# Performance work log

Measured on AMD Instinct MI355X. Metric: run time of the kernel, lower is better.

The kernel has to match this reference:

```python
import jax, jax.numpy as jnp
from jax import lax
import numpy as np

DN = ('NCHW', 'OIHW', 'NCHW')
NUM_CLASSES = 80
TOPK = 100
EPS = 1e-6


def seek_local_maximum(x, eps=EPS):
    # x: [b, c, h, w]; 8-neighbor local-max with zero padding, like the torch code
    xp = jnp.pad(x, ((0, 0), (0, 0), (1, 1), (1, 1)))
    m = ((x >= xp[:, :, :-2, 1:-1]) & (x >= xp[:, :, 2:, 1:-1])
         & (x >= xp[:, :, 1:-1, :-2]) & (x >= xp[:, :, 1:-1, 2:])
         & (x >= xp[:, :, :-2, :-2]) & (x >= xp[:, :, :-2, 2:])
         & (x >= xp[:, :, 2:, :-2]) & (x >= xp[:, :, 2:, 2:])
         & (x >= eps))
    return m.astype(x.dtype)


def setup_inputs() -> dict:
    key = jax.random.key(0)
    k1, k2, k3, k4 = jax.random.split(key, 4)
    b, c, h, w = 8, 256, 100, 152
    nc1 = NUM_CLASSES + 1
    x = jax.random.normal(k1, (b, c, h, w), dtype=jnp.float32)
    pos_embeddings = jax.random.normal(k2, (1, c, h, w), dtype=jnp.float32)
    w1 = jax.random.normal(k3, (c, c, 3, 3), dtype=jnp.float32) * 0.02
    b1 = jnp.zeros((c,), dtype=jnp.float32)
    w2 = jax.random.normal(k4, (nc1, c, 1, 1), dtype=jnp.float32) * 0.02
    b2 = jnp.zeros((nc1,), dtype=jnp.float32)
    return {"x": x, "pos_embeddings": pos_embeddings, "w1": w1, "b1": b1, "w2": w2, "b2": b2}


def reference(x, pos_embeddings, w1, b1, w2, b2):
    b, c, h, w = x.shape
    # conv 3x3 + relu + conv 1x1 -> class logits [b, nc+1, h, w]
    hid = lax.conv_general_dilated(x, w1, (1, 1), 'SAME', dimension_numbers=DN)
    hid = jax.nn.relu(hid + b1[None, :, None, None])
    logits = lax.conv_general_dilated(hid, w2, (1, 1), 'SAME', dimension_numbers=DN)
    logits = logits + b2[None, :, None, None]
    probs = jax.nn.softmax(logits, axis=1)
    # one-hot of argmax over foreground classes (excluding last 'no-object' channel)
    cls_idx = jnp.argmax(probs[:, :-1], axis=1)                    # [b, h, w]
    one_hot = jax.nn.one_hot(cls_idx, NUM_CLASSES + 1, dtype=probs.dtype)  # [b, h, w, nc+1]
    probs = probs * jnp.transpose(one_hot, (0, 3, 1, 2))
    probs = probs + seek_local_maximum(probs)
    # per-pixel foreground score, topk over spatial positions
    scores = jnp.max(probs[:, :-1], axis=1).reshape(b, h * w)      # [b, h*w]
    _, topk_idx = lax.top_k(scores, TOPK)                          # [b, topk]
    idx = topk_idx[:, None, :]                                     # [b, 1, topk]
    topk_proposals = jnp.take_along_axis(x.reshape(b, c, h * w), idx, axis=2)
    pos = jnp.broadcast_to(pos_embeddings, (b, c, h, w)).reshape(b, c, h * w)
    topk_pos_embeddings = jnp.take_along_axis(pos, idx, axis=2)
    # eval mode: topk_locations is None in the torch module; omit it
    return (topk_proposals, topk_pos_embeddings, logits)
```

## Files before the change

kernel.cpp:

```cpp
#include <hip/hip_runtime.h>
#include <hip/hip_bf16.h>

#define Hh    100
#define Ww    152
#define Pp    15200
#define Cc    256
#define NBATCH 8
#define NC1   81
#define NCLS  80
#define KTOP  100

#define PROWS 102
#define PCOLS 154
#define PIXB  1024
#define XT_BATCH_BYTES ((size_t)PROWS * PCOLS * PIXB)

typedef __attribute__((ext_vector_type(8))) short  bf16x8;
typedef __attribute__((ext_vector_type(4))) float  f32x4;

__device__ __forceinline__ unsigned short bf16_bits(float v) {
    __hip_bfloat16 h = __float2bfloat16(v);
    return *(unsigned short*)&h;
}
__device__ __forceinline__ float bf16_back(float v) {
    __hip_bfloat16 h = __float2bfloat16(v);
    return __bfloat162float(h);
}

typedef __attribute__((address_space(1))) const void GV;
typedef __attribute__((address_space(3))) void LV;
__device__ __forceinline__ void gload_lds16(const void* g, void* l) {
    __builtin_amdgcn_global_load_lds((GV*)g, (LV*)l, 16, 0, 0);
}

__global__ void pack_w(const float* __restrict__ w1, unsigned short* __restrict__ wpk)
{
    int id = blockIdx.x * 256 + threadIdx.x;
    int k = id >> 8, c = id & 255;
#pragma unroll
    for (int t = 0; t < 9; ++t) {
        float v = w1[(size_t)(k * 256 + c) * 9 + t];
        unsigned short hi = bf16_bits(v);
        unsigned short lo = bf16_bits(v - bf16_back(v));
        int region = ((c >> 5) * 9 + t) * 2;
        int base   = region * 8192;
        int pos    = (k >> 4) * 512 + ((c >> 3) & 3) * 128 + (k & 15) * 8 + (c & 7);
        wpk[base + pos]        = hi;
        wpk[base + 8192 + pos] = lo;
    }
}

__global__ void pack_w2t(const float* __restrict__ w2, float* __restrict__ w2t)
{
    int j = blockIdx.x;
    int c = threadIdx.x;
    float v = (j < NC1) ? w2[j * 256 + c] : 0.f;
    w2t[c * 84 + j] = v;
}

__global__ __launch_bounds__(256)
void pack_x(const float* __restrict__ x, unsigned short* __restrict__ xT)
{
    __shared__ float ls[64][257];
    const int tid   = threadIdx.x;
    const int chunk = blockIdx.x;
    const int row   = blockIdx.y;
    const int n     = blockIdx.z;
    const int c0    = chunk * 64;
    const int yy    = row - 1;
    const bool rowok = ((unsigned)yy < (unsigned)Hh);

    const int lanec = tid & 63;
    const int xx    = c0 + lanec - 1;
    const bool colok = ((unsigned)xx < (unsigned)Ww);
    const bool ok = rowok && colok;

    const size_t rbase = ((size_t)n * Cc) * Pp + (size_t)(rowok ? yy : 0) * Ww
                       + (size_t)(colok ? xx : 0);
#pragma unroll 4
    for (int i = 0; i < 64; ++i) {
        const int c = (tid >> 6) + i * 4;
        float v = 0.f;
        if (ok) v = x[rbase + (size_t)c * Pp];
        ls[lanec][c] = v;
    }
    __syncthreads();

    const int cch = tid;
    const int jmax = (c0 + 64 <= PCOLS) ? 64 : (PCOLS - c0);
#pragma unroll 4
    for (int j = 0; j < jmax; ++j) {
        const int pc = c0 + j;
        float v = ls[j][cch];
        unsigned short hi = bf16_bits(v);
        unsigned short lo = bf16_bits(v - bf16_back(v));
        size_t dst = (((size_t)n * PROWS + row) * PCOLS + pc) * 512 + cch;
        xT[dst]       = hi;
        xT[dst + 256] = lo;
    }
}

#define BBUFB 49152

#define MM(P,M,I,CUR) acc[M][I] = __builtin_amdgcn_mfma_f32_16x16x32_bf16( \
    (P)==2 ? al[CUR][M] : ah[CUR][M], (P)==1 ? bl[CUR][I] : bh[CUR][I], acc[M][I], 0, 0, 0);

#define CH0(C) MM(0,0,0,C) MM(0,0,1,C) MM(0,0,2,C) MM(0,0,3,C) MM(0,1,0,C) MM(0,1,1,C) \
               MM(0,1,2,C) MM(0,1,3,C) MM(0,2,0,C) MM(0,2,1,C) MM(0,2,2,C) MM(0,2,3,C)
#define CH1(C) MM(0,3,0,C) MM(0,3,1,C) MM(0,3,2,C) MM(0,3,3,C) MM(1,0,0,C) MM(1,0,1,C) \
               MM(1,0,2,C) MM(1,0,3,C) MM(1,1,0,C) MM(1,1,1,C) MM(1,1,2,C) MM(1,1,3,C)
#define CH2(C) MM(1,2,0,C) MM(1,2,1,C) MM(1,2,2,C) MM(1,2,3,C) MM(1,3,0,C) MM(1,3,1,C) \
               MM(1,3,2,C) MM(1,3,3,C) MM(2,0,0,C) MM(2,0,1,C) MM(2,0,2,C) MM(2,0,3,C)
#define CH3(C) MM(2,1,0,C) MM(2,1,1,C) MM(2,1,2,C) MM(2,1,3,C) MM(2,2,0,C) MM(2,2,1,C) \
               MM(2,2,2,C) MM(2,2,3,C) MM(2,3,0,C) MM(2,3,1,C) MM(2,3,2,C) MM(2,3,3,C)

#define SBAR __builtin_amdgcn_sched_barrier(0)

#define TAP(S,T,CUR,NX) { \
    const int U_  = (S) * 9 + (T); \
    const int un_ = (U_ + 1 < 72) ? U_ + 1 : 71; \
    loadAh(un_, ah[NX]); \
    SBAR; __builtin_amdgcn_s_setprio(1); CH0(CUR) __builtin_amdgcn_s_setprio(0); SBAR; \
    loadAl(un_, al[NX]); \
    SBAR; __builtin_amdgcn_s_setprio(1); CH1(CUR) __builtin_amdgcn_s_setprio(0); SBAR; \
    if ((T) < 8) readBh((S), (T) + 1, bh[NX]); \
    SBAR; __builtin_amdgcn_s_setprio(1); CH2(CUR) __builtin_amdgcn_s_setprio(0); SBAR; \
    if ((T) < 8) readBl((S), (T) + 1, bl[NX]); \
    SBAR; __builtin_amdgcn_s_setprio(1); CH3(CUR) __builtin_amdgcn_s_setprio(0); SBAR; \
}

#define TAPS_EVEN(S) TAP(S,0,0,1) TAP(S,1,1,0) TAP(S,2,0,1) TAP(S,3,1,0) TAP(S,4,0,1) \
                     TAP(S,5,1,0) TAP(S,6,0,1) TAP(S,7,1,0) TAP(S,8,0,1)
#define TAPS_ODD(S)  TAP(S,0,1,0) TAP(S,1,0,1) TAP(S,2,1,0) TAP(S,3,0,1) TAP(S,4,1,0) \
                     TAP(S,5,0,1) TAP(S,6,1,0) TAP(S,7,0,1) TAP(S,8,1,0)

__global__ __launch_bounds__(512, 2)
void conv3x3_mfma(const unsigned short* __restrict__ xT,
                  const unsigned short* __restrict__ wpk,
                  const float* __restrict__ b1, float* __restrict__ hid)
{
    __shared__ f32x4 ldsbuf[6144];
    char* L = (char*)ldsbuf;

    const int tid  = threadIdx.x;
    const int lane = tid & 63;
    const int wv   = tid >> 6;
    const int wm   = wv >> 2;
    const int wn   = wv & 3;
    const int quad = lane >> 4, lq = lane & 15;

    const int hwflat  = blockIdx.x + 65 * (blockIdx.y + 2 * blockIdx.z);
    const int logical = (hwflat & 7) * 130 + (hwflat >> 3);
    const int n   = logical / 130;
    const int rem = logical - n * 130;
    const int bx  = rem >> 1;
    const int k0b = rem & 1;

    const int rb = bx / 5, cb = bx - rb * 5;
    const int y0 = rb * 8;
    const int x0 = cb * 32;
    const int k0 = k0b * 128;

    const char* xb = (const char*)xT + (size_t)n * XT_BATCH_BYTES;
    const char* abase = (const char*)wpk + (size_t)(k0 >> 4) * 1024
                      + (size_t)(wm * 4) * 1024 + (size_t)lane * 16;

    const unsigned kslot = (lane & 7) ^ (lane >> 3);
    const size_t chnbase = (kslot < 4) ? (size_t)(kslot * 16)
                                       : (size_t)(448 + kslot * 16);

    auto stageB = [&](int s) {
        char* bdst = L + (size_t)(s & 1) * BBUFB;
        const size_t chn = (size_t)s * 64 + chnbase;
#pragma unroll
        for (int k6 = 0; k6 < 6; ++k6) {
            const int j   = wv + 8 * k6;
            const int pix = 8 * j + (lane >> 3);
            const int r   = pix / 34;
            const int c   = pix - r * 34;
            int prow = y0 + r; prow = prow < 102 ? prow : 101;
            const char* g = xb + (((size_t)(prow * 154 + x0 + c)) << 10) + chn;
            gload_lds16(g, bdst + (size_t)j * 1024);
        }
    };

    auto loadAh = [&](int u, bf16x8 (&a)[4]) {
        const char* p0 = abase + (size_t)u * 32768;
#pragma unroll
        for (int m = 0; m < 4; ++m) a[m] = *(const bf16x8*)(p0 + m * 1024);
    };
    auto loadAl = [&](int u, bf16x8 (&a)[4]) {
        const char* p0 = abase + (size_t)u * 32768 + 16384;
#pragma unroll
        for (int m = 0; m < 4; ++m) a[m] = *(const bf16x8*)(p0 + m * 1024);
    };

    const int pix0 = wn * 2 * 34 + lq;
    auto readBh = [&](int s, int t, bf16x8 (&b)[4]) {
        const char* Bb = L + (size_t)(s & 1) * BBUFB;
        const int ty = t / 3, tx = t - ty * 3;
        const int pb0 = pix0 + ty * 34 + tx;
#pragma unroll
        for (int i = 0; i < 4; ++i) {
            const int pix = pb0 + (i >> 1) * 34 + (i & 1) * 16;
            const int a = pix * 128 + ((quad ^ (pix & 7)) << 4);
            b[i] = *(const bf16x8*)(Bb + a);
        }
    };
    auto readBl = [&](int s, int t, bf16x8 (&b)[4]) {
        const char* Bb = L + (size_t)(s & 1) * BBUFB;
        const int ty = t / 3, tx = t - ty * 3;
        const int pb0 = pix0 + ty * 34 + tx;
#pragma unroll
        for (int i = 0; i < 4; ++i) {
            const int pix = pb0 + (i >> 1) * 34 + (i & 1) * 16;
            const int a = (pix * 128 + ((quad ^ (pix & 7)) << 4)) ^ 64;
            b[i] = *(const bf16x8*)(Bb + a);
        }
    };

    f32x4 acc[4][4];
#pragma unroll
    for (int a = 0; a < 4; ++a)
#pragma unroll
        for (int b = 0; b < 4; ++b) acc[a][b] = 0;

    bf16x8 ah[2][4], al[2][4], bh[2][4], bl[2][4];

    stageB(0);
    __syncthreads();
    loadAh(0, ah[0]); loadAl(0, al[0]);
    readBh(0, 0, bh[0]); readBl(0, 0, bl[0]);

#pragma unroll 1
    for (int sp = 0; sp < 4; ++sp) {
        const int s0 = sp * 2, s1 = s0 + 1;
        stageB(s0 + 1);
        TAPS_EVEN(s0)
        __syncthreads();
        readBh(s1, 0, bh[1]); readBl(s1, 0, bl[1]);
        if (s1 < 7) stageB(s1 + 1);
        TAPS_ODD(s1)
        __syncthreads();
        if (s1 < 7) { readBh(s1 + 1, 0, bh[0]); readBl(s1 + 1, 0, bl[0]); }
    }

#pragma unroll
    for (int m = 0; m < 4; ++m) {
        const int kb = k0 + wm * 64 + m * 16 + quad * 4;
        const float b0 = b1[kb], b1v = b1[kb + 1], b2v = b1[kb + 2], b3v = b1[kb + 3];
#pragma unroll
        for (int i = 0; i < 4; ++i) {
            const int y = y0 + wn * 2 + (i >> 1);
            const int xcol = x0 + (i & 1) * 16 + lq;
            if (y < Hh && xcol < Ww) {
                float* hp = hid + ((size_t)n * Cc + kb) * Pp + y * Ww + xcol;
                hp[0]              = fmaxf(acc[m][i].x + b0,  0.f);
                hp[Pp]             = fmaxf(acc[m][i].y + b1v, 0.f);
                hp[2 * Pp]         = fmaxf(acc[m][i].z + b2v, 0.f);
                hp[3 * (size_t)Pp] = fmaxf(acc[m][i].w + b3v, 0.f);
            }
        }
    }
}

__global__ __launch_bounds__(256, 2)
void conv1x1_softmax(const float* __restrict__ hid, const float* __restrict__ w2t,
                     const float* __restrict__ b2, float* __restrict__ logits,
                     float* __restrict__ pmap, int* __restrict__ cmap)
{
    const int tid = threadIdx.x;
    const int p   = blockIdx.x * 256 + tid;
    const int n   = blockIdx.y;
    const bool valid = (p < Pp);
    const int psafe = valid ? p : 0;

    float acc[84];
#pragma unroll
    for (int j = 0; j < 84; ++j) acc[j] = 0.f;

    const float* hptr = hid + ((size_t)n * Cc) * Pp + psafe;

    float h0 = hptr[0];
    float h1 = hptr[(size_t)Pp];
#pragma unroll 1
    for (int c = 0; c < Cc; ++c) {
        const int cn = (c + 2 < Cc) ? c + 2 : Cc - 1;
        const float hn = hptr[(size_t)cn * Pp];
        const float* wr = w2t + c * 84;
#pragma unroll
        for (int j = 0; j < 84; ++j) acc[j] = fmaf(wr[j], h0, acc[j]);
        h0 = h1; h1 = hn;
    }

    if (valid) {
#pragma unroll
        for (int j = 0; j < NC1; ++j) acc[j] += b2[j];

        float* lp = logits + (size_t)n * NC1 * Pp + p;
#pragma unroll
        for (int j = 0; j < NC1; ++j) lp[(size_t)j * Pp] = acc[j];

        float m = -3.4e38f;
#pragma unroll
        for (int j = 0; j < NC1; ++j) m = fmaxf(m, acc[j]);
        float s = 0.f;
#pragma unroll
        for (int j = 0; j < NC1; ++j) s += __expf(acc[j] - m);
        float best = -3.4e38f; int bi = 0;
#pragma unroll
        for (int j = 0; j < NCLS; ++j) {
            if (acc[j] > best) { best = acc[j]; bi = j; }
        }
        pmap[n * Pp + p] = __expf(best - m) / s;
        cmap[n * Pp + p] = bi;
    }
}

__global__ void local_score(const float* __restrict__ pmap, const int* __restrict__ cmap,
                            float* __restrict__ scores)
{
    int p = blockIdx.x * 256 + threadIdx.x;
    int n = blockIdx.y;
    if (p >= Pp) return;
    int base = n * Pp;
    float pv = pmap[base + p];
    int   c  = cmap[base + p];
    int y = p / Ww, xc = p - y * Ww;
    bool ok = (pv >= 1e-6f);
#pragma unroll
    for (int dy = -1; dy <= 1; ++dy)
#pragma unroll
        for (int dx = -1; dx <= 1; ++dx) {
            if (dy == 0 && dx == 0) continue;
            int yy = y + dy, xx = xc + dx;
            if (yy >= 0 && yy < Hh && xx >= 0 && xx < Ww) {
                int q = base + yy * Ww + xx;
                if (cmap[q] == c && pmap[q] > pv) ok = false;
            }
        }
    scores[base + p] = pv + (ok ? 1.f : 0.f);
}

__global__ __launch_bounds__(1024)
void topk_gather(const float* __restrict__ scores, const float* __restrict__ x,
                 const float* __restrict__ pos, float* __restrict__ oprop,
                 float* __restrict__ opos)
{
    __shared__ float sv[Pp];
    __shared__ int sidx[KTOP];
    __shared__ unsigned long long red[16];
    __shared__ unsigned long long bcast;
    const int tid = threadIdx.x;
    const int n   = blockIdx.x;

    for (int i = tid; i < Pp; i += 1024) sv[i] = scores[n * Pp + i];
    __syncthreads();

    auto scan = [&]() -> unsigned long long {
        unsigned long long best = 0ull;
#pragma unroll
        for (int k = 0; k < 15; ++k) {
            const int i = tid + k * 1024;
            if (i < Pp) {
                unsigned fb = __float_as_uint(sv[i]);
                unsigned long long key =
                    ((unsigned long long)fb << 32) | (unsigned)(0xFFFF - i);
                best = key > best ? key : best;
            }
        }
        return best;
    };

    unsigned long long mybest = scan();

    for (int it = 0; it < KTOP; ++it) {
        unsigned long long b = mybest;
#pragma unroll
        for (int off = 32; off > 0; off >>= 1) {
            unsigned long long o = __shfl_down(b, off, 64);
            b = o > b ? o : b;
        }
        if ((tid & 63) == 0) red[tid >> 6] = b;
        __syncthreads();
        if (tid == 0) {
            unsigned long long bf = red[0];
#pragma unroll
            for (int w = 1; w < 16; ++w) bf = red[w] > bf ? red[w] : bf;
            int idx = 0xFFFF - (int)(bf & 0xFFFFFFFFull);
            sidx[it] = idx;
            sv[idx]  = 0.f;
            bcast    = bf;
        }
        __syncthreads();
        const unsigned long long w = bcast;
        const int idx = 0xFFFF - (int)(w & 0xFFFFFFFFull);
        if ((idx & 1023) == tid) mybest = scan();
    }

    for (int t = tid; t < Cc * KTOP; t += 1024) {
        int c = t / KTOP;
        int i = t - c * KTOP;
        int idx = sidx[i];
        oprop[n * Cc * KTOP + c * KTOP + i] = x[((size_t)n * Cc + c) * Pp + idx];
        opos [n * Cc * KTOP + c * KTOP + i] = pos[(size_t)c * Pp + idx];
    }
}

extern "C" void kernel_launch(void* const* d_in, const int* in_sizes, int n_in,
                              void* d_out, int out_size, void* d_ws, size_t ws_size,
                              hipStream_t stream)
{
    const float* x   = (const float*)d_in[0];
    const float* pos = (const float*)d_in[1];
    const float* w1  = (const float*)d_in[2];
    const float* b1  = (const float*)d_in[3];
    const float* w2  = (const float*)d_in[4];
    const float* b2  = (const float*)d_in[5];

    float* out    = (float*)d_out;
    float* oprop  = out;
    float* oposE  = out + (size_t)NBATCH * Cc * KTOP;
    float* logits = out + (size_t)2 * NBATCH * Cc * KTOP;

    unsigned short* wpk = (unsigned short*)logits;

    float* ws  = (float*)d_ws;
    float* hid = ws;
    unsigned short* xT = (unsigned short*)(ws + (size_t)NBATCH * Cc * Pp);
    char* after_xt = (char*)xT + (size_t)NBATCH * XT_BATCH_BYTES;
    float* pmap   = (float*)after_xt;
    int*   cmap   = (int*)(pmap + (size_t)NBATCH * Pp);
    float* scores = (float*)(cmap + (size_t)NBATCH * Pp);
    float* w2t    = scores + (size_t)NBATCH * Pp;

    pack_w<<<256, 256, 0, stream>>>(w1, wpk);
    pack_w2t<<<84, 256, 0, stream>>>(w2, w2t);
    pack_x<<<dim3(3, PROWS, NBATCH), 256, 0, stream>>>(x, xT);
    conv3x3_mfma<<<dim3(65, 2, NBATCH), 512, 0, stream>>>(
        xT, wpk, b1, hid);
    conv1x1_softmax<<<dim3((Pp + 255) / 256, NBATCH), 256, 0, stream>>>(
        hid, w2t, b2, logits, pmap, cmap);
    local_score<<<dim3((Pp + 255) / 256, NBATCH), 256, 0, stream>>>(
        pmap, cmap, scores);
    topk_gather<<<NBATCH, 1024, 0, stream>>>(scores, x, pos, oprop, oposE);
}
```

Before: 1.117 ms.

## Stage 1x1 conv weights in LDS and compute two pixels per thread

The separate w2 transpose kernel is removed. The 1x1 conv kernel now loads 64-channel slices of w2 into shared memory in transposed form and reads them as float4. Each thread computes two pixels with 168 accumulators, halving the block size, so every weight read serves two outputs. This is meant to cut global/scalar weight-load traffic and a kernel launch, but the higher register pressure may cause spills or lower occupancy.

```diff
diff --git a/kernel.cpp b/kernel.cpp
--- a/kernel.cpp
+++ b/kernel.cpp
@@ -48,14 +48,6 @@
         wpk[base + pos]        = hi;
         wpk[base + 8192 + pos] = lo;
     }
-}
-
-__global__ void pack_w2t(const float* __restrict__ w2, float* __restrict__ w2t)
-{
-    int j = blockIdx.x;
-    int c = threadIdx.x;
-    float v = (j < NC1) ? w2[j * 256 + c] : 0.f;
-    w2t[c * 84 + j] = v;
 }
 
 __global__ __launch_bounds__(256)
@@ -264,36 +256,62 @@
     }
 }
 
-__global__ __launch_bounds__(256, 2)
-void conv1x1_softmax(const float* __restrict__ hid, const float* __restrict__ w2t,
+__global__ __launch_bounds__(128, 2)
+void conv1x1_softmax(const float* __restrict__ hid, const float* __restrict__ w2,
                      const float* __restrict__ b2, float* __restrict__ logits,
                      float* __restrict__ pmap, int* __restrict__ cmap)
 {
+    __shared__ float w2s[64 * 84];
     const int tid = threadIdx.x;
-    const int p   = blockIdx.x * 256 + tid;
+    const int p0  = blockIdx.x * 256 + tid;
+    const int p1  = p0 + 128;
     const int n   = blockIdx.y;
-    const bool valid = (p < Pp);
-    const int psafe = valid ? p : 0;
-
-    float acc[84];
-#pragma unroll
-    for (int j = 0; j < 84; ++j) acc[j] = 0.f;
-
-    const float* hptr = hid + ((size_t)n * Cc) * Pp + psafe;
-
-    float h0 = hptr[0];
-    float h1 = hptr[(size_t)Pp];
+    const bool v0 = (p0 < Pp), v1 = (p1 < Pp);
+    const int ps0 = v0 ? p0 : 0;
+    const int ps1 = v1 ? p1 : 0;
+
+    float acca[84], accb[84];
+#pragma unroll
+    for (int j = 0; j < 84; ++j) { acca[j] = 0.f; accb[j] = 0.f; }
+
 #pragma unroll 1
-    for (int c = 0; c < Cc; ++c) {
-        const int cn = (c + 2 < Cc) ? c + 2 : Cc - 1;
-        const float hn = hptr[(size_t)cn * Pp];
-        const float* wr = w2t + c * 84;
-#pragma unroll
-        for (int j = 0; j < 84; ++j) acc[j] = fmaf(wr[j], h0, acc[j]);
-        h0 = h1; h1 = hn;
-    }
-
-    if (valid) {
+    for (int c0 = 0; c0 < Cc; c0 += 64) {
+        __syncthreads();
+#pragma unroll
+        for (int i = 0; i < 42; ++i) {
+            int q  = i * 128 + tid;
+            int cl = q / 84;
+            int j  = q - cl * 84;
+            float v = 0.f;
+            if (j < NC1) v = w2[j * 256 + c0 + cl];
+            w2s[cl * 84 + j] = v;
+        }
+        __syncthreads();
+
+        const float* h0p = hid + ((size_t)n * Cc + c0) * Pp + ps0;
+        const float* h1p = hid + ((size_t)n * Cc + c0) * Pp + ps1;
+#pragma unroll 2
+        for (int cl = 0; cl < 64; ++cl) {
+            float ha = h0p[(size_t)cl * Pp];
+            float hb = h1p[(size_t)cl * Pp];
+            const float4* wrow = (const float4*)(&w2s[cl * 84]);
+#pragma unroll
+            for (int f = 0; f < 21; ++f) {
+                float4 wv = wrow[f];
+                acca[f * 4 + 0] = fmaf(wv.x, ha, acca[f * 4 + 0]);
+                acca[f * 4 + 1] = fmaf(wv.y, ha, acca[f * 4 + 1]);
+                acca[f * 4 + 2] = fmaf(wv.z, ha, acca[f * 4 + 2]);
+                acca[f * 4 + 3] = fmaf(wv.w, ha, acca[f * 4 + 3]);
+                accb[f * 4 + 0] = fmaf(wv.x, hb, accb[f * 4 + 0]);
+                accb[f * 4 + 1] = fmaf(wv.y, hb, accb[f * 4 + 1]);
+                accb[f * 4 + 2] = fmaf(wv.z, hb, accb[f * 4 + 2]);
+                accb[f * 4 + 3] = fmaf(wv.w, hb, accb[f * 4 + 3]);
+            }
+        }
+    }
+
+    auto finish = [&](bool valid, int p, float (&acc)[84]) {
+        if (!valid) return;
 #pragma unroll
         for (int j = 0; j < NC1; ++j) acc[j] += b2[j];
 
@@ -314,7 +332,9 @@
         }
         pmap[n * Pp + p] = __expf(best - m) / s;
         cmap[n * Pp + p] = bi;
-    }
+    };
+    finish(v0, p0, acca);
+    finish(v1, p1, accb);
 }
 
 __global__ void local_score(const float* __restrict__ pmap, const int* __restrict__ cmap,
@@ -432,15 +452,13 @@
     float* pmap   = (float*)after_xt;
     int*   cmap   = (int*)(pmap + (size_t)NBATCH * Pp);
     float* scores = (float*)(cmap + (size_t)NBATCH * Pp);
-    float* w2t    = scores + (size_t)NBATCH * Pp;
 
     pack_w<<<256, 256, 0, stream>>>(w1, wpk);
-    pack_w2t<<<84, 256, 0, stream>>>(w2, w2t);
     pack_x<<<dim3(3, PROWS, NBATCH), 256, 0, stream>>>(x, xT);
     conv3x3_mfma<<<dim3(65, 2, NBATCH), 512, 0, stream>>>(
         xT, wpk, b1, hid);
-    conv1x1_softmax<<<dim3((Pp + 255) / 256, NBATCH), 256, 0, stream>>>(
-        hid, w2t, b2, logits, pmap, cmap);
+    conv1x1_softmax<<<dim3((Pp + 255) / 256, NBATCH), 128, 0, stream>>>(
+        hid, w2, b2, logits, pmap, cmap);
     local_score<<<dim3((Pp + 255) / 256, NBATCH), 256, 0, stream>>>(
         pmap, cmap, scores);
     topk_gather<<<NBATCH, 1024, 0, stream>>>(scores, x, pos, oprop, oposE);
```

After: 1.345 ms. +20.4%, slower.
